# Optimization experiments

Measured on AMD Instinct MI355X. Metric: run time of the kernel, lower is better.

The kernel has to match this reference:

```python
import jax, jax.numpy as jnp
import numpy as np

B, T, H = 32, 512, 1024   # batch, seq, hidden
L = 512                   # max_seq_length (must be <= 512 for rel_pos_bias)
E = 2048                  # hidden * expansion_factor
S = 128                   # shared qk dim
SQRT_S = float(np.sqrt(S))
EPS = 1e-5


def setup_inputs() -> dict:
    key = jax.random.key(0)
    ks = jax.random.split(key, 9)
    return {
        "x": jax.random.normal(ks[0], (B, T, H), jnp.float32),
        "ln_w": jnp.ones((H,), jnp.float32),
        "ln_b": jnp.zeros((H,), jnp.float32),
        "uv_w": jax.random.normal(ks[1], (2 * E + S, H), jnp.float32) * 0.02,  # torch Linear [out,in]
        "uv_b": jnp.zeros((2 * E + S,), jnp.float32),
        "gamma": jax.random.uniform(ks[2], (2, S), jnp.float32),
        "beta": jax.random.uniform(ks[3], (2, S), jnp.float32),
        "w": jax.random.uniform(ks[4], (2 * L - 1,), jnp.float32),  # Toeplitz rel-pos table
        "o_w": jax.random.normal(ks[5], (H, E), jnp.float32) * 0.02,
        "o_b": jnp.zeros((H,), jnp.float32),
    }


def _rope(x):
    # x: [B, T, 2, S]; positions run along the seq dim (dim=1), faithful to GAU.rope
    half = x.shape[-1] // 2
    pos = jnp.arange(x.shape[1], dtype=x.dtype)
    # note: original uses 10000**(+i/half) (increasing freq) — keep it faithful
    inv_freq = 10000.0 ** (jnp.arange(half, dtype=x.dtype) / half)
    sinusoid = pos[:, None] * inv_freq[None, :]          # [T, half]
    sin = jnp.sin(sinusoid)[None, :, None, :]            # [1, T, 1, half]
    cos = jnp.cos(sinusoid)[None, :, None, :]
    x1, x2 = jnp.split(x, 2, axis=-1)
    return jnp.concatenate([x1 * cos - x2 * sin, x2 * cos + x1 * sin], axis=-1)


def reference(x, ln_w, ln_b, uv_w, uv_b, gamma, beta, w, o_w, o_b):
    Tq = x.shape[1]
    shortcut = x  # hidden_size == output_size -> residual
    # LayerNorm
    mu = jnp.mean(x, axis=-1, keepdims=True)
    var = jnp.mean(jnp.square(x - mu), axis=-1, keepdims=True)
    xn = (x - mu) / jnp.sqrt(var + EPS) * ln_w + ln_b
    # fused uv projection + SiLU, then split into gate u, value v, base
    uv = jax.nn.silu(xn @ uv_w.T + uv_b)                  # [B, T, 2E+S]
    u, v, base = uv[..., :E], uv[..., E:2 * E], uv[..., 2 * E:]
    base = base[:, :, None, :] * gamma[None, None] + beta  # [B, T, 2, S]
    base = _rope(base)
    q, k = base[:, :, 0, :], base[:, :, 1, :]             # [B, T, S]
    qk = jnp.einsum('bis,bjs->bij', q, k)                 # [B, T, T]
    # Toeplitz rel-pos bias: bias[i, j] = w[j - i + L - 1]
    rel = jnp.arange(Tq)[None, :] - jnp.arange(Tq)[:, None] + (L - 1)
    bias = w[rel]                                         # [T, T]
    kernel = jnp.square(jax.nn.relu(qk / SQRT_S + bias[None]))  # squared-ReLU attention
    out = u * jnp.einsum('bij,bje->bie', kernel, v)       # gated attention output [B, T, E]
    return out @ o_w.T + o_b + shortcut
```

## Files before the change

kernel.cpp:

```cpp
#include <hip/hip_runtime.h>

typedef unsigned short u16;
typedef __bf16 bf16x8 __attribute__((ext_vector_type(8)));
typedef float f32x4 __attribute__((ext_vector_type(4)));

#define B_ 32
#define T_ 512
#define H_ 1024
#define E_ 2048
#define S_ 128

__device__ inline u16 f2bf(float f) {
  union { float f; unsigned int u; } c; c.f = f;
  unsigned int u = c.u;
  unsigned int r = (u + 0x7FFFu + ((u >> 16) & 1u)) >> 16;
  return (u16)r;
}
__device__ inline float bf2f(u16 h) {
  union { unsigned int u; float f; } c; c.u = ((unsigned int)h) << 16; return c.f;
}
__device__ inline float silu_fast(float v) {
  return v * __builtin_amdgcn_rcpf(1.0f + __expf(-v));
}

__device__ inline void g2lds16(const u16* g, u16* l) {
  __builtin_amdgcn_global_load_lds(
      (const __attribute__((address_space(1))) void*)g,
      (__attribute__((address_space(3))) void*)l, 16, 0, 0);
}

__global__ __launch_bounds__(256) void ln_kernel(const float* __restrict__ x,
                                                 const float* __restrict__ lw,
                                                 const float* __restrict__ lb,
                                                 u16* __restrict__ xn) {
  int row = blockIdx.x;
  int t = threadIdx.x;
  const float4* xr = (const float4*)(x + (size_t)row * H_);
  float4 v = xr[t];
  float s = v.x + v.y + v.z + v.w;
  float ss = v.x * v.x + v.y * v.y + v.z * v.z + v.w * v.w;
  for (int off = 1; off < 64; off <<= 1) {
    s += __shfl_xor(s, off);
    ss += __shfl_xor(ss, off);
  }
  __shared__ float red[8];
  int w = t >> 6, l = t & 63;
  if (l == 0) { red[w] = s; red[4 + w] = ss; }
  __syncthreads();
  s = red[0] + red[1] + red[2] + red[3];
  ss = red[4] + red[5] + red[6] + red[7];
  float mu = s * (1.0f / H_);
  float var = ss * (1.0f / H_) - mu * mu;
  float inv = rsqrtf(var + 1e-5f);
  int i = t * 4;
  ushort4 o;
  o.x = f2bf((v.x - mu) * inv * lw[i] + lb[i]);
  o.y = f2bf((v.y - mu) * inv * lw[i + 1] + lb[i + 1]);
  o.z = f2bf((v.z - mu) * inv * lw[i + 2] + lb[i + 2]);
  o.w = f2bf((v.w - mu) * inv * lw[i + 3] + lb[i + 3]);
  *(ushort4*)(xn + (size_t)row * H_ + i) = o;
}

__global__ void cvt_kernel(const float* __restrict__ in, u16* __restrict__ out, int n4) {
  int i = blockIdx.x * 256 + threadIdx.x;
  if (i < n4) {
    float4 v = ((const float4*)in)[i];
    ushort4 o;
    o.x = f2bf(v.x); o.y = f2bf(v.y); o.z = f2bf(v.z); o.w = f2bf(v.w);
    ((ushort4*)out)[i] = o;
  }
}

__global__ __launch_bounds__(256) void rope_kernel(const float* __restrict__ base,
                                                   const float* __restrict__ gamma,
                                                   const float* __restrict__ beta,
                                                   u16* __restrict__ q,
                                                   u16* __restrict__ k) {
  int row = blockIdx.x * 4 + (threadIdx.x >> 6);
  int s = threadIdx.x & 63;
  int t = row & (T_ - 1);
  const float* bp = base + (size_t)row * S_;
  float b1 = bp[s], b2 = bp[s + 64];
  float q1 = b1 * gamma[s] + beta[s];
  float q2 = b2 * gamma[64 + s] + beta[64 + s];
  float k1 = b1 * gamma[128 + s] + beta[128 + s];
  float k2 = b2 * gamma[192 + s] + beta[192 + s];
  float invf = (float)pow(10000.0, (double)s * (1.0 / 64.0));
  float ph = (float)t * invf;
  float sn, cs;
  sincosf(ph, &sn, &cs);
  size_t o = (size_t)row * S_;
  q[o + s]      = f2bf(q1 * cs - q2 * sn);
  q[o + 64 + s] = f2bf(q2 * cs + q1 * sn);
  k[o + s]      = f2bf(k1 * cs - k2 * sn);
  k[o + 64 + s] = f2bf(k2 * cs + k1 * sn);
}

template <int MODE>
__global__ __launch_bounds__(256)
void gemm_bt(const u16* __restrict__ A, const u16* __restrict__ Bm,
             int K, long long sA, long long sB,
             void* __restrict__ o0, void* __restrict__ o1, void* __restrict__ o2,
             const void* __restrict__ c0, const void* __restrict__ c1, int nb0) {
  __shared__ __attribute__((aligned(16))) u16 lds[32768];
  u16* lsA = lds;
  u16* lsB = lds + 16384;

  const int z = blockIdx.z;
  const u16* Ab = A + (long long)z * sA;
  const u16* Bb = Bm + (long long)z * sB;
  const int m0 = blockIdx.y * 128;
  const int n0 = nb0 + blockIdx.x * 128;
  const int t = threadIdx.x;
  const int w = t >> 6, l = t & 63;
  const int quad = l >> 4, l16 = l & 15;
  const int wm = (w >> 1) * 64, wn = (w & 1) * 64;
  const int srow = t >> 4;
  const int gl = (t & 15) ^ ((t >> 4) & 7);
  const int dst_off = t * 8;
  const int rsw = l16 & 7;

  f32x4 zero = {0.f, 0.f, 0.f, 0.f};
  f32x4 acc[4][4];
  for (int mi = 0; mi < 4; ++mi)
    for (int ni = 0; ni < 4; ++ni) acc[mi][ni] = zero;

  const u16* gA = Ab + ((size_t)(m0 + srow) * K + gl * 8);
  const u16* gB = Bb + ((size_t)(n0 + srow) * K + gl * 8);
  const size_t rK16 = (size_t)16 * K;

  for (int k0 = 0; k0 < K; k0 += 128) {
    __syncthreads();
#pragma unroll
    for (int c = 0; c < 8; ++c)
      g2lds16(gA + k0 + c * rK16, &lsA[c * 2048 + dst_off]);
#pragma unroll
    for (int c = 0; c < 8; ++c)
      g2lds16(gB + k0 + c * rK16, &lsB[c * 2048 + dst_off]);
    __syncthreads();
#pragma unroll
    for (int j = 0; j < 4; ++j) {
      int pg = ((j * 4 + quad) ^ rsw) * 8;
      bf16x8 af[4], bfr[4];
      for (int i = 0; i < 4; ++i) {
        af[i]  = *(const bf16x8*)&lsA[(wm + i * 16 + l16) * 128 + pg];
        bfr[i] = *(const bf16x8*)&lsB[(wn + i * 16 + l16) * 128 + pg];
      }
      for (int mi = 0; mi < 4; ++mi)
        for (int ni = 0; ni < 4; ++ni)
          acc[mi][ni] = __builtin_amdgcn_mfma_f32_16x16x32_bf16(af[mi], bfr[ni], acc[mi][ni], 0, 0, 0);
    }
  }

  if constexpr (MODE == 0) {
    const float* uvb = (const float*)c0;
    if (n0 < E_) {
      for (int mi = 0; mi < 4; ++mi)
        for (int ni = 0; ni < 4; ++ni) {
          int n = n0 + wn + ni * 16 + l16;
          float bias = uvb[n];
          for (int r = 0; r < 4; ++r) {
            int m = m0 + wm + mi * 16 + quad * 4 + r;
            ((u16*)o0)[(size_t)m * E_ + n] = f2bf(silu_fast(acc[mi][ni][r] + bias));
          }
        }
    } else if (n0 < 2 * E_) {
      const int bb = m0 >> 9;
      const int tt0 = m0 & (T_ - 1);
      const int nv0 = n0 - E_;
      for (int h = 0; h < 2; ++h) {
        __syncthreads();
        if ((w & 1) == h) {
          for (int mi = 0; mi < 4; ++mi)
            for (int ni = 0; ni < 4; ++ni) {
              int nl = ni * 16 + l16;
              float bias = uvb[n0 + h * 64 + nl];
              for (int r = 0; r < 4; ++r) {
                int ml = wm + mi * 16 + quad * 4 + r;
                u16 sv = f2bf(silu_fast(acc[mi][ni][r] + bias));
                int g = ml >> 3, o = ml & 7;
                int gs = g ^ (nl & 7);
                lds[nl * 128 + gs * 8 + o] = sv;
              }
            }
        }
        __syncthreads();
        int row = t >> 2;
        int q4 = t & 3;
        size_t gbase = ((size_t)bb * E_ + nv0 + h * 64 + row) * T_ + tt0;
        for (int gg = 0; gg < 4; ++gg) {
          int g = q4 * 4 + gg;
          int gsw = g ^ (row & 7);
          uint4 val = *(const uint4*)&lds[row * 128 + gsw * 8];
          *(uint4*)&(((u16*)o1)[gbase + g * 8]) = val;
        }
      }
    } else {
      for (int mi = 0; mi < 4; ++mi)
        for (int ni = 0; ni < 4; ++ni) {
          int n = n0 + wn + ni * 16 + l16;
          float bias = uvb[n];
          for (int r = 0; r < 4; ++r) {
            int m = m0 + wm + mi * 16 + quad * 4 + r;
            ((float*)o2)[(size_t)m * S_ + (n - 2 * E_)] = silu_fast(acc[mi][ni][r] + bias);
          }
        }
    }
  } else {
    for (int mi = 0; mi < 4; ++mi) {
      for (int ni = 0; ni < 4; ++ni) {
        int n = n0 + wn + ni * 16 + l16;
        for (int r = 0; r < 4; ++r) {
          int m = m0 + wm + mi * 16 + quad * 4 + r;
          float a = acc[mi][ni][r];
          if constexpr (MODE == 1) {
            const float* wrel = (const float*)c0;
            float v = a * 0.08838834764831845f + wrel[n - m + 511];
            v = fmaxf(v, 0.0f);
            ((u16*)o0)[(size_t)z * (T_ * T_) + (size_t)m * T_ + n] = f2bf(v * v);
          } else if constexpr (MODE == 2) {
            const u16* uu = (const u16*)c0;
            size_t gi = ((size_t)z * T_ + m) * E_ + n;
            float uv_ = bf2f(uu[gi]);
            ((u16*)o0)[gi] = f2bf(a * uv_);
          } else {
            const float* ob = (const float*)c0;
            const float* xs = (const float*)c1;
            size_t gi = (size_t)m * H_ + n;
            ((float*)o0)[gi] = a + ob[n] + xs[gi];
          }
        }
      }
    }
  }
}

#define PH_SYNC()                                        \
  asm volatile("s_waitcnt lgkmcnt(0)" ::: "memory");     \
  __builtin_amdgcn_sched_barrier(0);                     \
  __builtin_amdgcn_s_barrier();                          \
  __builtin_amdgcn_sched_barrier(0);                     \
  __builtin_amdgcn_s_setprio(1);

#define PH_END()                                         \
  __builtin_amdgcn_s_setprio(0);

#define MM2(mA, mB)                                                                                       \
  _Pragma("unroll")                                                                                       \
  for (int ni = 0; ni < 4; ++ni) {                                                                        \
    acc[mA][ni] = __builtin_amdgcn_mfma_f32_16x16x32_bf16(af[mA][0], bfr[ni][0], acc[mA][ni], 0, 0, 0);   \
    acc[mB][ni] = __builtin_amdgcn_mfma_f32_16x16x32_bf16(af[mB][0], bfr[ni][0], acc[mB][ni], 0, 0, 0);   \
  }                                                                                                       \
  _Pragma("unroll")                                                                                       \
  for (int ni = 0; ni < 4; ++ni) {                                                                        \
    acc[mA][ni] = __builtin_amdgcn_mfma_f32_16x16x32_bf16(af[mA][1], bfr[ni][1], acc[mA][ni], 0, 0, 0);   \
    acc[mB][ni] = __builtin_amdgcn_mfma_f32_16x16x32_bf16(af[mB][1], bfr[ni][1], acc[mB][ni], 0, 0, 0);   \
  }

template <int MODE, bool XSWZ>
__global__ __launch_bounds__(512, 2)
void gemm256(const u16* __restrict__ A, const u16* __restrict__ Bm,
             int K, long long sA, long long sB,
             void* __restrict__ o0, void* __restrict__ o1,
             const void* __restrict__ c0, const void* __restrict__ c1) {
  extern __shared__ u16 lds[];

  int bx = blockIdx.x, by = blockIdx.y;
  if constexpr (XSWZ) {
    int gx = gridDim.x;
    int nwg = gx * gridDim.y;
    int hh = by * gx + bx;
    int cpx = nwg >> 3;
    int lid = (hh & 7) * cpx + (hh >> 3);
    bx = lid % gx; by = lid / gx;
  }
  const int z = blockIdx.z;
  const u16* Ab = A + (long long)z * sA;
  const u16* Bb = Bm + (long long)z * sB;
  const int m0 = by * 256;
  const int n0 = bx * 256;
  const int t = threadIdx.x;
  const int w = t >> 6, ln = t & 63;
  const int quad = ln >> 4, l16 = ln & 15;
  const int wm = w >> 2, wn = w & 3;

  const int nkt = K >> 6;

  const int goff = ((t & 7) ^ ((t >> 3) & 7)) * 8;
  const u16* gA = Ab + (size_t)(m0 + (t >> 3)) * K + goff;
  const u16* gB = Bb + (size_t)(n0 + (t >> 3)) * K + goff;
  u16* ldst = lds + t * 8;
  const size_t rK64 = (size_t)64 * K;
  const size_t rK128 = (size_t)128 * K;

  auto SA = [&](int b, int h, int kt) {
    const u16* g = gA + h * rK128 + (size_t)kt * 64;
    u16* d = ldst + b * 16384 + h * 8192;
    g2lds16(g, d);
    g2lds16(g + rK64, d + 4096);
  };
  auto SB = [&](int b, int h, int kt) {
    const u16* g = gB + h * rK128 + (size_t)kt * 64;
    u16* d = ldst + 32768 + b * 16384 + h * 8192;
    g2lds16(g, d);
    g2lds16(g + rK64, d + 4096);
  };

  f32x4 zero = {0.f, 0.f, 0.f, 0.f};
  f32x4 acc[8][4];
#pragma unroll
  for (int mi = 0; mi < 8; ++mi)
#pragma unroll
    for (int ni = 0; ni < 4; ++ni) acc[mi][ni] = zero;

  SA(0, 0, 0); SA(0, 1, 0); SB(0, 0, 0); SB(0, 1, 0);
  if (nkt > 1) {
    SB(1, 0, 1); SB(1, 1, 1); SA(1, 0, 1);
    asm volatile("s_waitcnt vmcnt(6)" ::: "memory");
  } else {
    asm volatile("s_waitcnt vmcnt(0)" ::: "memory");
  }
  __builtin_amdgcn_s_barrier();

  const u16* lA0 = lds + wm * 8192 + l16 * 64;
  const u16* lB0 = lds + 32768 + (wn >> 1) * 8192 + ((wn & 1) * 64 + l16) * 64;
  const int pg0 = (quad ^ (l16 & 7)) * 8;
  const int pg1 = ((4 + quad) ^ (l16 & 7)) * 8;

  bf16x8 bfr[4][2];
  bf16x8 af[8][2];

  for (int kt = 0; kt < nkt; ++kt) {
    const int b = kt & 1;
    const u16* lA = lA0 + b * 16384;
    const u16* lB = lB0 + b * 16384;
    const bool s2 = (kt + 2 < nkt);

#pragma unroll
    for (int ni = 0; ni < 4; ++ni) {
      bfr[ni][0] = *(const bf16x8*)&lB[ni * 1024 + pg0];
      bfr[ni][1] = *(const bf16x8*)&lB[ni * 1024 + pg1];
    }
#pragma unroll
    for (int mi = 0; mi < 2; ++mi) {
      af[mi][0] = *(const bf16x8*)&lA[mi * 1024 + pg0];
      af[mi][1] = *(const bf16x8*)&lA[mi * 1024 + pg1];
    }
    if (kt + 1 < nkt) SA(b ^ 1, 1, kt + 1);
    PH_SYNC();
    MM2(0, 1);
    PH_END();

#pragma unroll
    for (int mi = 2; mi < 6; ++mi) {
      af[mi][0] = *(const bf16x8*)&lA[mi * 1024 + pg0];
      af[mi][1] = *(const bf16x8*)&lA[mi * 1024 + pg1];
    }
    if (s2) SB(b, 0, kt + 2);
    PH_SYNC();
    MM2(2, 3);
    PH_END();

#pragma unroll
    for (int mi = 6; mi < 8; ++mi) {
      af[mi][0] = *(const bf16x8*)&lA[mi * 1024 + pg0];
      af[mi][1] = *(const bf16x8*)&lA[mi * 1024 + pg1];
    }
    if (s2) SB(b, 1, kt + 2);
    PH_SYNC();
    MM2(4, 5);
    PH_END();

    if (s2) {
      SA(b, 0, kt + 2);
      asm volatile("s_waitcnt vmcnt(6)" ::: "memory");
    } else {
      asm volatile("s_waitcnt vmcnt(0)" ::: "memory");
    }
    __builtin_amdgcn_sched_barrier(0);
    __builtin_amdgcn_s_barrier();
    __builtin_amdgcn_sched_barrier(0);
    __builtin_amdgcn_s_setprio(1);
    MM2(6, 7);
    PH_END();
  }

  if constexpr (MODE == 0) {
    const float* uvb = (const float*)c0;
    if (n0 < E_) {
#pragma unroll
      for (int ni = 0; ni < 4; ++ni) {
        int n = n0 + wn * 64 + ni * 16 + l16;
        float bias = uvb[n];
#pragma unroll
        for (int mi = 0; mi < 8; ++mi)
#pragma unroll
          for (int r = 0; r < 4; ++r) {
            int m = m0 + wm * 128 + mi * 16 + quad * 4 + r;
            ((u16*)o0)[(size_t)m * E_ + n] = f2bf(silu_fast(acc[mi][ni][r] + bias));
          }
      }
    } else {
      const int bb = m0 >> 9;
      const int tt0 = m0 & (T_ - 1);
      const int nv0 = n0 - E_;
#pragma unroll
      for (int ni = 0; ni < 4; ++ni) {
        int nl = wn * 64 + ni * 16 + l16;
        float bias = uvb[n0 + nl];
#pragma unroll
        for (int mi = 0; mi < 8; ++mi)
#pragma unroll
          for (int r = 0; r < 4; ++r) {
            int ml = wm * 128 + mi * 16 + quad * 4 + r;
            u16 sv = f2bf(silu_fast(acc[mi][ni][r] + bias));
            int g = ml >> 3, o = ml & 7;
            lds[nl * 256 + ((g ^ (nl & 7)) << 3) + o] = sv;
          }
      }
      __syncthreads();
      int row = t >> 1;
      u16* o1p = (u16*)o1;
      size_t gbase = ((size_t)bb * E_ + nv0 + row) * T_ + tt0;
#pragma unroll
      for (int cc = 0; cc < 16; ++cc) {
        int c = (t & 1) * 16 + cc;
        int gs = c ^ (row & 7);
        uint4 val = *(const uint4*)&lds[row * 256 + gs * 8];
        *(uint4*)&o1p[gbase + c * 8] = val;
      }
    }
  } else if constexpr (MODE == 2) {
    const u16* uu = (const u16*)c0;
#pragma unroll
    for (int mi = 0; mi < 8; ++mi)
#pragma unroll
      for (int ni = 0; ni < 4; ++ni) {
        int n = n0 + wn * 64 + ni * 16 + l16;
#pragma unroll
        for (int r = 0; r < 4; ++r) {
          int m = m0 + wm * 128 + mi * 16 + quad * 4 + r;
          size_t gi = ((size_t)z * T_ + m) * E_ + n;
          float uv_ = bf2f(uu[gi]);
          ((u16*)o0)[gi] = f2bf(acc[mi][ni][r] * uv_);
        }
      }
  } else {
    const float* ob = (const float*)c0;
    const float* xs = (const float*)c1;
#pragma unroll
    for (int ni = 0; ni < 4; ++ni) {
      int n = n0 + wn * 64 + ni * 16 + l16;
      float bias = ob[n];
#pragma unroll
      for (int mi = 0; mi < 8; ++mi)
#pragma unroll
        for (int r = 0; r < 4; ++r) {
          int m = m0 + wm * 128 + mi * 16 + quad * 4 + r;
          size_t gi = (size_t)m * H_ + n;
          ((float*)o0)[gi] = acc[mi][ni][r] + bias + xs[gi];
        }
    }
  }
}

extern "C" void kernel_launch(void* const* d_in, const int* in_sizes, int n_in,
                              void* d_out, int out_size, void* d_ws, size_t ws_size,
                              hipStream_t stream) {
  const float* x     = (const float*)d_in[0];
  const float* ln_w  = (const float*)d_in[1];
  const float* ln_b  = (const float*)d_in[2];
  const float* uv_w  = (const float*)d_in[3];
  const float* uv_b  = (const float*)d_in[4];
  const float* gamma = (const float*)d_in[5];
  const float* beta  = (const float*)d_in[6];
  const float* wrel  = (const float*)d_in[7];
  const float* o_w   = (const float*)d_in[8];
  const float* o_b   = (const float*)d_in[9];

  char* ws = (char*)d_ws;
  u16*   xn   = (u16*)(ws);
  u16*   qb   = (u16*)(ws);
  u16*   kb   = (u16*)(ws + 4194304);
  u16*   km   = (u16*)(ws + 8388608);
  u16*   uvwb = (u16*)(ws + 33554432);
  u16*   owb  = (u16*)(ws + 42205184);
  u16*   u    = (u16*)(ws + 46399488);
  u16*   vt   = (u16*)(ws + 113508352);
  float* base = (float*)(ws + 180617216);
  u16*   attn = u;

  static int use256 = -1;
  if (use256 < 0) {
    auto* k0 = gemm256<0, true>;
    auto* k2 = gemm256<2, false>;
    auto* k3 = gemm256<3, true>;
    hipError_t e0 = hipFuncSetAttribute((const void*)k0, hipFuncAttributeMaxDynamicSharedMemorySize, 131072);
    hipError_t e2 = hipFuncSetAttribute((const void*)k2, hipFuncAttributeMaxDynamicSharedMemorySize, 131072);
    hipError_t e3 = hipFuncSetAttribute((const void*)k3, hipFuncAttributeMaxDynamicSharedMemorySize, 131072);
    use256 = (e0 == hipSuccess && e2 == hipSuccess && e3 == hipSuccess) ? 1 : 0;
  }

  ln_kernel<<<16384, 256, 0, stream>>>(x, ln_w, ln_b, xn);
  cvt_kernel<<<4224, 256, 0, stream>>>(uv_w, uvwb, 4224 * 1024 / 4);
  cvt_kernel<<<2048, 256, 0, stream>>>(o_w, owb, 1024 * 2048 / 4);

  if (use256) {
    gemm256<0, true><<<dim3(16, 64, 1), 512, 131072, stream>>>(
        xn, uvwb, 1024, 0, 0, u, vt, uv_b, nullptr);
    gemm_bt<0><<<dim3(1, 128, 1), 256, 0, stream>>>(
        xn, uvwb, 1024, 0, 0, u, vt, base, uv_b, nullptr, 4096);
    rope_kernel<<<4096, 256, 0, stream>>>(base, gamma, beta, qb, kb);
    gemm_bt<1><<<dim3(4, 4, 32), 256, 0, stream>>>(
        qb, kb, 128, 65536, 65536, km, nullptr, nullptr, wrel, nullptr, 0);
    gemm256<2, false><<<dim3(8, 2, 32), 512, 131072, stream>>>(
        km, vt, 512, 262144, 1048576, attn, nullptr, u, nullptr);
    gemm256<3, true><<<dim3(4, 64, 1), 512, 131072, stream>>>(
        attn, owb, 2048, 0, 0, d_out, nullptr, o_b, x);
  } else {
    gemm_bt<0><<<dim3(33, 128, 1), 256, 0, stream>>>(
        xn, uvwb, 1024, 0, 0, u, vt, base, uv_b, nullptr, 0);
    rope_kernel<<<4096, 256, 0, stream>>>(base, gamma, beta, qb, kb);
    gemm_bt<1><<<dim3(4, 4, 32), 256, 0, stream>>>(
        qb, kb, 128, 65536, 65536, km, nullptr, nullptr, wrel, nullptr, 0);
    gemm_bt<2><<<dim3(16, 4, 32), 256, 0, stream>>>(
        km, vt, 512, 262144, 1048576, attn, nullptr, nullptr, u, nullptr, 0);
    gemm_bt<3><<<dim3(8, 128, 1), 256, 0, stream>>>(
        attn, owb, 2048, 0, 0, d_out, nullptr, nullptr, o_b, x, 0);
  }
}
```

Measured before the change: 535.6 us.

## Restructure GEMM main loop into two phases with coarser prefetch staging

The 256-tile GEMM inner loop goes from four barrier-separated phases of 2 M-fragments each to two phases of 4 M-fragments each. Both A halves for the next k-tile are issued in the first phase and both B halves for k+2 in the second, with vmcnt thresholds adjusted to match. This halves the barriers and priority switches per k-iteration and gives longer MFMA runs. The cost is less interleaving of global loads with compute, and all of A must land in a shorter window, which could expose load latency.

```diff
diff --git a/kernel.cpp b/kernel.cpp
--- a/kernel.cpp
+++ b/kernel.cpp
@@ -245,16 +245,20 @@
 #define PH_END()                                         \
   __builtin_amdgcn_s_setprio(0);
 
-#define MM2(mA, mB)                                                                                       \
-  _Pragma("unroll")                                                                                       \
-  for (int ni = 0; ni < 4; ++ni) {                                                                        \
-    acc[mA][ni] = __builtin_amdgcn_mfma_f32_16x16x32_bf16(af[mA][0], bfr[ni][0], acc[mA][ni], 0, 0, 0);   \
-    acc[mB][ni] = __builtin_amdgcn_mfma_f32_16x16x32_bf16(af[mB][0], bfr[ni][0], acc[mB][ni], 0, 0, 0);   \
-  }                                                                                                       \
-  _Pragma("unroll")                                                                                       \
-  for (int ni = 0; ni < 4; ++ni) {                                                                        \
-    acc[mA][ni] = __builtin_amdgcn_mfma_f32_16x16x32_bf16(af[mA][1], bfr[ni][1], acc[mA][ni], 0, 0, 0);   \
-    acc[mB][ni] = __builtin_amdgcn_mfma_f32_16x16x32_bf16(af[mB][1], bfr[ni][1], acc[mB][ni], 0, 0, 0);   \
+#define MM4(mb)                                                                                                   \
+  _Pragma("unroll")                                                                                               \
+  for (int ni = 0; ni < 4; ++ni) {                                                                                \
+    acc[mb + 0][ni] = __builtin_amdgcn_mfma_f32_16x16x32_bf16(af[mb + 0][0], bfr[ni][0], acc[mb + 0][ni], 0, 0, 0); \
+    acc[mb + 1][ni] = __builtin_amdgcn_mfma_f32_16x16x32_bf16(af[mb + 1][0], bfr[ni][0], acc[mb + 1][ni], 0, 0, 0); \
+    acc[mb + 2][ni] = __builtin_amdgcn_mfma_f32_16x16x32_bf16(af[mb + 2][0], bfr[ni][0], acc[mb + 2][ni], 0, 0, 0); \
+    acc[mb + 3][ni] = __builtin_amdgcn_mfma_f32_16x16x32_bf16(af[mb + 3][0], bfr[ni][0], acc[mb + 3][ni], 0, 0, 0); \
+  }                                                                                                               \
+  _Pragma("unroll")                                                                                               \
+  for (int ni = 0; ni < 4; ++ni) {                                                                                \
+    acc[mb + 0][ni] = __builtin_amdgcn_mfma_f32_16x16x32_bf16(af[mb + 0][1], bfr[ni][1], acc[mb + 0][ni], 0, 0, 0); \
+    acc[mb + 1][ni] = __builtin_amdgcn_mfma_f32_16x16x32_bf16(af[mb + 1][1], bfr[ni][1], acc[mb + 1][ni], 0, 0, 0); \
+    acc[mb + 2][ni] = __builtin_amdgcn_mfma_f32_16x16x32_bf16(af[mb + 2][1], bfr[ni][1], acc[mb + 2][ni], 0, 0, 0); \
+    acc[mb + 3][ni] = __builtin_amdgcn_mfma_f32_16x16x32_bf16(af[mb + 3][1], bfr[ni][1], acc[mb + 3][ni], 0, 0, 0); \
   }
 
 template <int MODE, bool XSWZ>
@@ -315,8 +319,8 @@
 
   SA(0, 0, 0); SA(0, 1, 0); SB(0, 0, 0); SB(0, 1, 0);
   if (nkt > 1) {
-    SB(1, 0, 1); SB(1, 1, 1); SA(1, 0, 1);
-    asm volatile("s_waitcnt vmcnt(6)" ::: "memory");
+    SB(1, 0, 1); SB(1, 1, 1);
+    asm volatile("s_waitcnt vmcnt(4)" ::: "memory");
   } else {
     asm volatile("s_waitcnt vmcnt(0)" ::: "memory");
   }
@@ -330,11 +334,10 @@
   bf16x8 bfr[4][2];
   bf16x8 af[8][2];
 
-  for (int kt = 0; kt < nkt; ++kt) {
-    const int b = kt & 1;
+  for (int j = 0; j < nkt; ++j) {
+    const int b = j & 1;
     const u16* lA = lA0 + b * 16384;
     const u16* lB = lB0 + b * 16384;
-    const bool s2 = (kt + 2 < nkt);
 
 #pragma unroll
     for (int ni = 0; ni < 4; ++ni) {
@@ -342,46 +345,33 @@
       bfr[ni][1] = *(const bf16x8*)&lB[ni * 1024 + pg1];
     }
 #pragma unroll
-    for (int mi = 0; mi < 2; ++mi) {
+    for (int mi = 0; mi < 4; ++mi) {
       af[mi][0] = *(const bf16x8*)&lA[mi * 1024 + pg0];
       af[mi][1] = *(const bf16x8*)&lA[mi * 1024 + pg1];
     }
-    if (kt + 1 < nkt) SA(b ^ 1, 1, kt + 1);
+    if (j + 1 < nkt) { SA(b ^ 1, 0, j + 1); SA(b ^ 1, 1, j + 1); }
     PH_SYNC();
-    MM2(0, 1);
+    MM4(0);
     PH_END();
 
 #pragma unroll
-    for (int mi = 2; mi < 6; ++mi) {
+    for (int mi = 4; mi < 8; ++mi) {
       af[mi][0] = *(const bf16x8*)&lA[mi * 1024 + pg0];
       af[mi][1] = *(const bf16x8*)&lA[mi * 1024 + pg1];
     }
-    if (s2) SB(b, 0, kt + 2);
-    PH_SYNC();
-    MM2(2, 3);
-    PH_END();
-
-#pragma unroll
-    for (int mi = 6; mi < 8; ++mi) {
-      af[mi][0] = *(const bf16x8*)&lA[mi * 1024 + pg0];
-      af[mi][1] = *(const bf16x8*)&lA[mi * 1024 + pg1];
-    }
-    if (s2) SB(b, 1, kt + 2);
-    PH_SYNC();
-    MM2(4, 5);
-    PH_END();
-
-    if (s2) {
-      SA(b, 0, kt + 2);
-      asm volatile("s_waitcnt vmcnt(6)" ::: "memory");
+    if (j + 2 < nkt) {
+      SB(b, 0, j + 2); SB(b, 1, j + 2);
+      asm volatile("s_waitcnt lgkmcnt(0)" ::: "memory");
+      asm volatile("s_waitcnt vmcnt(4)" ::: "memory");
     } else {
+      asm volatile("s_waitcnt lgkmcnt(0)" ::: "memory");
       asm volatile("s_waitcnt vmcnt(0)" ::: "memory");
     }
     __builtin_amdgcn_sched_barrier(0);
     __builtin_amdgcn_s_barrier();
     __builtin_amdgcn_sched_barrier(0);
     __builtin_amdgcn_s_setprio(1);
-    MM2(6, 7);
+    MM4(4);
     PH_END();
   }
 
```

Result: no change. 528.5 us (-1.3%).
